# Performance work log

Measured on AMD Instinct MI355X. Metric: run time of the kernel, lower is better.

Reference implementation:

```python
import jax, jax.numpy as jnp
import numpy as np

VOCAB = 50257
EMB = 1024
HID = 1024
B, T = 8, 256


def setup_inputs() -> dict:
    key = jax.random.key(0)
    ks = jax.random.split(key, 6)
    s = 0.05  # small init scale for numerical sanity
    return {
        "x": jax.random.randint(ks[0], (B, T), 0, VOCAB, dtype=jnp.int64) if jax.config.jax_enable_x64 else jax.random.randint(ks[0], (B, T), 0, VOCAB, dtype=jnp.int32),
        "emb_W": jax.random.normal(ks[1], (VOCAB, EMB), dtype=jnp.float32) * s,
        "W_ih": jax.random.normal(ks[2], (4 * HID, EMB), dtype=jnp.float32) * s,
        "W_hh": jax.random.normal(ks[3], (4 * HID, HID), dtype=jnp.float32) * s,
        "b_ih": jax.random.normal(ks[4], (4 * HID,), dtype=jnp.float32) * s,
        "b_hh": jax.random.normal(ks[5], (4 * HID,), dtype=jnp.float32) * s,
        "dec_b": jnp.zeros((VOCAB,), dtype=jnp.float32),
    }


def _lstm(emb, W_ih, W_hh, b_ih, b_hh):
    # emb: [B, T, E]. Precompute input projections for all timesteps (one big GEMM).
    x_proj = jnp.einsum("bte,ge->btg", emb, W_ih) + (b_ih + b_hh)  # [B, T, 4H]
    h0 = jnp.zeros((emb.shape[0], HID), emb.dtype)
    c0 = jnp.zeros((emb.shape[0], HID), emb.dtype)

    def step(carry, xt):  # xt: [B, 4H]
        h, c = carry
        g = xt + h @ W_hh.T  # [B, 4H]
        i, f, gg, o = jnp.split(g, 4, axis=-1)  # PyTorch gate order i,f,g,o
        i = jax.nn.sigmoid(i)
        f = jax.nn.sigmoid(f)
        gg = jnp.tanh(gg)
        o = jax.nn.sigmoid(o)
        c_new = f * c + i * gg
        h_new = o * jnp.tanh(c_new)
        return (h_new, c_new), h_new

    (hT, cT), hs = jax.lax.scan(step, (h0, c0), jnp.swapaxes(x_proj, 0, 1))
    out = jnp.swapaxes(hs, 0, 1)  # [B, T, H], batch_first
    return out, (hT[None], cT[None])  # num_layers=1 leading dim


def reference(x, emb_W, W_ih, W_hh, b_ih, b_hh, dec_b):
    emb = emb_W[x]                                   # [B, T, E]
    out, hidden = _lstm(emb, W_ih, W_hh, b_ih, b_hh)  # [B, T, H]
    logits = jnp.einsum("bth,vh->btv", out, emb_W) + dec_b  # tied decoder
    logits = logits.reshape(-1, VOCAB)
    return jax.nn.log_softmax(logits, axis=1), hidden
```

## Files before the change

### kernel.cpp

```cpp
#include <hip/hip_runtime.h>

typedef float f32x4 __attribute__((ext_vector_type(4)));
typedef __bf16 bf16x8 __attribute__((ext_vector_type(8)));
typedef unsigned int u32x4 __attribute__((ext_vector_type(4)));
typedef unsigned short u16;
typedef unsigned int u32;

#define VOCAB 50257
#define KDIM 1024
#define MROWS 2048
#define TSEQ 256
#define NBLK 64
#define NTILE 393
#define NT (NTILE * 2)
#define LOGN ((size_t)MROWS * VOCAB)

__device__ __forceinline__ u16 f2bf(float f) {
    u32 u = __builtin_bit_cast(u32, f);
    u = (u + 0x7FFFu + ((u >> 16) & 1u)) >> 16;
    return (u16)u;
}

__device__ __forceinline__ float sigm(float x) { return 1.0f / (1.0f + __expf(-x)); }

__device__ __forceinline__ u32 min4u(u32x4 v) {
    u32 a = v.x < v.y ? v.x : v.y;
    u32 b = v.z < v.w ? v.z : v.w;
    return a < b ? a : b;
}


__global__ void conv_bf16(const float4* __restrict__ in, ushort4* __restrict__ out, long n4) {
    long i = (long)blockIdx.x * blockDim.x + threadIdx.x;
    long stride = (long)gridDim.x * blockDim.x;
    for (; i < n4; i += stride) {
        float4 v = in[i];
        ushort4 o;
        o.x = f2bf(v.x); o.y = f2bf(v.y); o.z = f2bf(v.z); o.w = f2bf(v.w);
        out[i] = o;
    }
}

__global__ void bias_sum(const float* __restrict__ a, const float* __restrict__ b,
                         float* __restrict__ o) {
    int i = blockIdx.x * 256 + threadIdx.x;
    if (i < 4096) o[i] = a[i] + b[i];
}

__global__ __launch_bounds__(256) void gather_emb(const int* __restrict__ x,
                                                  const float* __restrict__ embW,
                                                  u16* __restrict__ out) {
    int m = blockIdx.x;
    int row = x[m];
    const float4* src = (const float4*)(embW + (size_t)row * KDIM);
    ushort4* dst = (ushort4*)(out + (size_t)m * KDIM);
    float4 v = src[threadIdx.x];
    ushort4 o;
    o.x = f2bf(v.x); o.y = f2bf(v.y); o.z = f2bf(v.z); o.w = f2bf(v.w);
    dst[threadIdx.x] = o;
}

__global__ void init_hseq(u32* __restrict__ hs) {
    int i = blockIdx.x * 256 + threadIdx.x;
    if (i < 257 * 4096) hs[i] = (i < 4096) ? 0x00010001u : 0u;
}


#define BM 128
#define BN 128
#define BK 64

__device__ __forceinline__ void gl_lds16(const u16* g, const u16* l) {
    __builtin_amdgcn_global_load_lds(
        (const __attribute__((address_space(1))) u32*)g,
        (__attribute__((address_space(3))) u32*)l, 16, 0, 0);
}

__global__ __launch_bounds__(256, 2)
void gemm_bt(const u16* __restrict__ A, const u16* __restrict__ Bm,
             const float* __restrict__ bias, float* __restrict__ C,
             int N, int Nb, int K, int ldc)
{
    __shared__ __align__(16) u16 As[BM * BK];
    __shared__ __align__(16) u16 Bs[BN * BK];
    const int tid  = threadIdx.x;
    const int lane = tid & 63;
    const int wid  = tid >> 6;

    const int gx  = gridDim.x;
    const int nwg = gx * gridDim.y;
    const int lin = blockIdx.y * gx + blockIdx.x;
    const int qq = nwg >> 3, rr = nwg & 7;
    const int xcd = lin & 7, idx = lin >> 3;
    const int neu = (xcd < rr) ? (xcd * (qq + 1) + idx)
                               : (rr * (qq + 1) + (xcd - rr) * qq + idx);
    const int bm = neu % gx;
    const int bn = neu / gx;

    const int wr = wid >> 1, wc = wid & 1;

    const u16* gA[4]; const u16* gB[4];
    const u16* ldsA[4]; const u16* ldsB[4];
#pragma unroll
    for (int r = 0; r < 4; ++r) {
        int L = r * 256 + tid;
        int row = L >> 3, ps = L & 7;
        int ls = ps ^ (row & 7);
        gA[r] = A + (size_t)(bm * BM + row) * K + ls * 8;
        int brow = bn * BN + row; brow = brow < Nb ? brow : Nb - 1;
        gB[r] = Bm + (size_t)brow * K + ls * 8;
        ldsA[r] = As + (r * 256 + wid * 64) * 8;
        ldsB[r] = Bs + (r * 256 + wid * 64) * 8;
    }

    const int lrow = lane & 15, ksl = lane >> 4;
    int aoff[4][2], boff[4][2];
#pragma unroll
    for (int i = 0; i < 4; ++i)
#pragma unroll
        for (int ks = 0; ks < 2; ++ks) {
            int ar = wr * 64 + i * 16 + lrow;
            aoff[i][ks] = ar * BK + (((ks * 4 + ksl) ^ (ar & 7)) * 8);
            int br = wc * 64 + i * 16 + lrow;
            boff[i][ks] = br * BK + (((ks * 4 + ksl) ^ (br & 7)) * 8);
        }

    f32x4 acc[4][4] = {};
    for (int kt = 0; kt < K; kt += BK) {
#pragma unroll
        for (int r = 0; r < 4; ++r) gl_lds16(gA[r] + kt, ldsA[r]);
#pragma unroll
        for (int r = 0; r < 4; ++r) gl_lds16(gB[r] + kt, ldsB[r]);
        __syncthreads();
        bf16x8 af[4][2], bfb[4][2];
#pragma unroll
        for (int i = 0; i < 4; ++i)
#pragma unroll
            for (int ks = 0; ks < 2; ++ks) {
                af[i][ks]  = *(const bf16x8*)(As + aoff[i][ks]);
                bfb[i][ks] = *(const bf16x8*)(Bs + boff[i][ks]);
            }
#pragma unroll
        for (int ks = 0; ks < 2; ++ks)
#pragma unroll
            for (int mi = 0; mi < 4; ++mi)
#pragma unroll
                for (int ni = 0; ni < 4; ++ni)
                    acc[mi][ni] = __builtin_amdgcn_mfma_f32_16x16x32_bf16(
                        af[mi][ks], bfb[ni][ks], acc[mi][ni], 0, 0, 0);
        __syncthreads();
    }

    const int crl = lane >> 4, ccl = lane & 15;
    const int row0 = bm * BM + wr * 64, col0 = bn * BN + wc * 64;
#pragma unroll
    for (int ni = 0; ni < 4; ++ni) {
        int col = col0 + ni * 16 + ccl;
        if (col < N) {
            float bv = bias[col];
#pragma unroll
            for (int mi = 0; mi < 4; ++mi) {
                int row = row0 + mi * 16 + crl * 4;
                float* cp = C + (size_t)row * ldc + col;
#pragma unroll
                for (int r = 0; r < 4; ++r)
                    cp[(size_t)r * ldc] = acc[mi][ni][r] + bv;
            }
        }
    }
}


__global__ __launch_bounds__(256, 2)
void gemm_dec(const u16* __restrict__ A, const u16* __restrict__ Bm,
              const float* __restrict__ bias, float* __restrict__ C,
              float* __restrict__ pmax, float* __restrict__ psum)
{
    const int N = VOCAB, Nb = VOCAB, K = KDIM, ldc = VOCAB;
    __shared__ __align__(16) u16 As[BM * BK];
    __shared__ __align__(16) u16 Bs[BN * BK];
    const int tid  = threadIdx.x;
    const int lane = tid & 63;
    const int wid  = tid >> 6;

    const int gx  = gridDim.x;
    const int nwg = gx * gridDim.y;
    const int lin = blockIdx.y * gx + blockIdx.x;
    const int qq = nwg >> 3, rr = nwg & 7;
    const int xcd = lin & 7, idx = lin >> 3;
    const int neu = (xcd < rr) ? (xcd * (qq + 1) + idx)
                               : (rr * (qq + 1) + (xcd - rr) * qq + idx);
    const int bm = neu % gx;
    const int bn = neu / gx;

    const int wr = wid >> 1, wc = wid & 1;

    const u16* gA[4]; const u16* gB[4];
    const u16* ldsA[4]; const u16* ldsB[4];
#pragma unroll
    for (int r = 0; r < 4; ++r) {
        int L = r * 256 + tid;
        int row = L >> 3, ps = L & 7;
        int ls = ps ^ (row & 7);
        gA[r] = A + (size_t)(bm * BM + row) * K + ls * 8;
        int brow = bn * BN + row; brow = brow < Nb ? brow : Nb - 1;
        gB[r] = Bm + (size_t)brow * K + ls * 8;
        ldsA[r] = As + (r * 256 + wid * 64) * 8;
        ldsB[r] = Bs + (r * 256 + wid * 64) * 8;
    }

    const int lrow = lane & 15, ksl = lane >> 4;
    int aoff[4][2], boff[4][2];
#pragma unroll
    for (int i = 0; i < 4; ++i)
#pragma unroll
        for (int ks = 0; ks < 2; ++ks) {
            int ar = wr * 64 + i * 16 + lrow;
            aoff[i][ks] = ar * BK + (((ks * 4 + ksl) ^ (ar & 7)) * 8);
            int br = wc * 64 + i * 16 + lrow;
            boff[i][ks] = br * BK + (((ks * 4 + ksl) ^ (br & 7)) * 8);
        }

    f32x4 acc[4][4] = {};
    for (int kt = 0; kt < K; kt += BK) {
#pragma unroll
        for (int r = 0; r < 4; ++r) gl_lds16(gA[r] + kt, ldsA[r]);
#pragma unroll
        for (int r = 0; r < 4; ++r) gl_lds16(gB[r] + kt, ldsB[r]);
        __syncthreads();
        bf16x8 af[4][2], bfb[4][2];
#pragma unroll
        for (int i = 0; i < 4; ++i)
#pragma unroll
            for (int ks = 0; ks < 2; ++ks) {
                af[i][ks]  = *(const bf16x8*)(As + aoff[i][ks]);
                bfb[i][ks] = *(const bf16x8*)(Bs + boff[i][ks]);
            }
#pragma unroll
        for (int ks = 0; ks < 2; ++ks)
#pragma unroll
            for (int mi = 0; mi < 4; ++mi)
#pragma unroll
                for (int ni = 0; ni < 4; ++ni)
                    acc[mi][ni] = __builtin_amdgcn_mfma_f32_16x16x32_bf16(
                        af[mi][ks], bfb[ni][ks], acc[mi][ni], 0, 0, 0);
        __syncthreads();
    }

    const int crl = lane >> 4, ccl = lane & 15;
    const int row0 = bm * BM + wr * 64, col0 = bn * BN + wc * 64;
    float bve[4]; bool vld[4];
#pragma unroll
    for (int ni = 0; ni < 4; ++ni) {
        int col = col0 + ni * 16 + ccl;
        vld[ni] = col < N;
        bve[ni] = vld[ni] ? bias[col] : 0.f;
    }
#pragma unroll
    for (int ni = 0; ni < 4; ++ni) {
        if (vld[ni]) {
            int col = col0 + ni * 16 + ccl;
#pragma unroll
            for (int mi = 0; mi < 4; ++mi) {
                int row = row0 + mi * 16 + crl * 4;
                float* cp = C + (size_t)row * ldc + col;
#pragma unroll
                for (int r = 0; r < 4; ++r)
                    cp[(size_t)r * ldc] = acc[mi][ni][r] + bve[ni];
            }
        }
    }
#pragma unroll
    for (int mi = 0; mi < 4; ++mi)
#pragma unroll
        for (int r = 0; r < 4; ++r) {
            int row = row0 + mi * 16 + crl * 4 + r;
            float v0 = vld[0] ? acc[mi][0][r] + bve[0] : -3.0e38f;
            float v1 = vld[1] ? acc[mi][1][r] + bve[1] : -3.0e38f;
            float v2 = vld[2] ? acc[mi][2][r] + bve[2] : -3.0e38f;
            float v3 = vld[3] ? acc[mi][3][r] + bve[3] : -3.0e38f;
            float rmax = fmaxf(fmaxf(v0, v1), fmaxf(v2, v3));
#pragma unroll
            for (int m2 = 1; m2 < 16; m2 <<= 1) rmax = fmaxf(rmax, __shfl_xor(rmax, m2));
            float rs = __expf(v0 - rmax) + __expf(v1 - rmax) +
                       __expf(v2 - rmax) + __expf(v3 - rmax);
#pragma unroll
            for (int m2 = 1; m2 < 16; m2 <<= 1) rs += __shfl_xor(rs, m2);
            if (ccl == 0) {
                pmax[(size_t)row * NT + bn * 2 + wc] = rmax;
                psum[(size_t)row * NT + bn * 2 + wc] = rs;
            }
        }
}


__global__ __launch_bounds__(256, 1)
void lstm_persist(const u16* __restrict__ Whh,
                  const float* __restrict__ xproj,
                  u16* __restrict__ hseq,
                  u16* __restrict__ hall,
                  float* __restrict__ outTail)
{
    const int tid  = threadIdx.x;
    const int lane = tid & 63;
    const int wq   = tid >> 6;
    const int lrow = lane & 15, ksl = lane >> 4;
    const int bid  = blockIdx.x;
    const int colbase = bid * 16;

    bf16x8 Bf[32];
    {
        const u16* bp = Whh + (size_t)(wq * 1024 + colbase + lrow) * KDIM + ksl * 8;
#pragma unroll
        for (int kk = 0; kk < 32; ++kk)
            asm volatile("global_load_dwordx4 %0, %1, off"
                         : "=v"(Bf[kk]) : "v"(bp + kk * 32));
        asm volatile("s_waitcnt vmcnt(0)" ::: "memory");
        __builtin_amdgcn_sched_barrier(0);
    }

    __shared__ float S[4][8][16];
    __shared__ __align__(16) u16 hstage[2][64][16][16];

    for (int i = tid; i < 2 * 64 * 8; i += 256) {
        int buf = i >> 9, rem = i & 511;
        int j = rem >> 3, row = 8 + (rem & 7);
        u32x4 z = {0, 0, 0, 0};
        *(u32x4*)(&hstage[buf][j][row][0]) = z;
        *(u32x4*)(&hstage[buf][j][row][8]) = z;
    }

    const bool upd = tid < 128;
    const int b8 = tid >> 4, c16 = tid & 15;
    float creg = 0.f;
    float xp0 = 0.f, xp1 = 0.f, xp2 = 0.f, xp3 = 0.f;
    size_t xbase = 0;
    if (upd) {
        xbase = (size_t)b8 * TSEQ * 4096 + colbase + c16;
        xp0 = xproj[xbase];          xp1 = xproj[xbase + 1024];
        xp2 = xproj[xbase + 2048];   xp3 = xproj[xbase + 3072];
    }

    const int pj = tid >> 2, pr = (tid & 3) * 2;
    const int abase = (ksl >> 1) * 256 + lrow * 16 + (ksl & 1) * 8;

    for (int t = 0; t < TSEQ; ++t) {
        const u32* src = (const u32*)hseq + (size_t)t * 4096 + pj * 64 + pr * 8;
        u32x4 P0, P1, P2, P3;
        for (;;) {
            asm volatile("global_load_dwordx4 %0, %1, off sc0 sc1" : "=v"(P0) : "v"(src));
            asm volatile("global_load_dwordx4 %0, %1, off sc0 sc1" : "=v"(P1) : "v"(src + 4));
            asm volatile("global_load_dwordx4 %0, %1, off sc0 sc1" : "=v"(P2) : "v"(src + 8));
            asm volatile("global_load_dwordx4 %0, %1, off sc0 sc1" : "=v"(P3) : "v"(src + 12));
            asm volatile("s_waitcnt vmcnt(0)" ::: "memory");
            __builtin_amdgcn_sched_barrier(0);
            u32 a = min4u(P0), b = min4u(P1), c = min4u(P2), d = min4u(P3);
            u32 mn = (a < b ? a : b); u32 mn2 = (c < d ? c : d);
            if ((mn < mn2 ? mn : mn2) != 0u) break;
        }
        {
            u16* dst = &hstage[t & 1][pj][pr][0];
            *(u32x4*)(dst)      = P0;
            *(u32x4*)(dst + 8)  = P1;
            *(u32x4*)(dst + 16) = P2;
            *(u32x4*)(dst + 24) = P3;
        }
        __syncthreads();

        const u16* sb = &hstage[t & 1][0][0][0] + abase;
        f32x4 ac0 = {}, ac1 = {}, ac2 = {}, ac3 = {};
#pragma unroll
        for (int g = 0; g < 8; ++g) {
            bf16x8 a0 = *(const bf16x8*)(sb + (size_t)(g * 4 + 0) * 512);
            bf16x8 a1 = *(const bf16x8*)(sb + (size_t)(g * 4 + 1) * 512);
            bf16x8 a2 = *(const bf16x8*)(sb + (size_t)(g * 4 + 2) * 512);
            bf16x8 a3 = *(const bf16x8*)(sb + (size_t)(g * 4 + 3) * 512);
            ac0 = __builtin_amdgcn_mfma_f32_16x16x32_bf16(a0, Bf[g * 4 + 0], ac0, 0, 0, 0);
            ac1 = __builtin_amdgcn_mfma_f32_16x16x32_bf16(a1, Bf[g * 4 + 1], ac1, 0, 0, 0);
            ac2 = __builtin_amdgcn_mfma_f32_16x16x32_bf16(a2, Bf[g * 4 + 2], ac2, 0, 0, 0);
            ac3 = __builtin_amdgcn_mfma_f32_16x16x32_bf16(a3, Bf[g * 4 + 3], ac3, 0, 0, 0);
        }
        if (ksl < 2) {
#pragma unroll
            for (int r = 0; r < 4; ++r)
                S[wq][ksl * 4 + r][lrow] = ac0[r] + ac1[r] + ac2[r] + ac3[r];
        }
        __syncthreads();

        if (upd) {
            float gi = S[0][b8][c16] + xp0;
            float gf = S[1][b8][c16] + xp1;
            float gg = S[2][b8][c16] + xp2;
            float go = S[3][b8][c16] + xp3;
            float iv = sigm(gi), fv = sigm(gf), ov = sigm(go);
            float gv = tanhf(gg);
            creg = fv * creg + iv * gv;
            float hv = ov * tanhf(creg);
            u16 hbx = f2bf(hv) | 1;
            int w0 = (int)hbx;
            int w1 = __shfl_down(w0, 1);
            if (!(c16 & 1)) {
                u32 w = (u32)(u16)w0 | ((u32)(u16)w1 << 16);
                u32* dst = (u32*)hseq + (size_t)(t + 1) * 4096 + bid * 64 + b8 * 8 + (c16 >> 1);
                __hip_atomic_store(dst, w, __ATOMIC_RELAXED, __HIP_MEMORY_SCOPE_AGENT);
            }
            hall[((size_t)b8 * TSEQ + t) * KDIM + colbase + c16] = hbx;
            if (t == TSEQ - 1) {
                outTail[b8 * KDIM + colbase + c16] = hv;
                outTail[8192 + b8 * KDIM + colbase + c16] = creg;
            }
            int tn = (t + 1 < TSEQ) ? t + 1 : t;
            size_t xb = xbase + (size_t)tn * 4096;
            xp0 = xproj[xb];        xp1 = xproj[xb + 1024];
            xp2 = xproj[xb + 2048]; xp3 = xproj[xb + 3072];
        }
    }
}


__global__ __launch_bounds__(256)
void merge_lse(const float* __restrict__ pmax, const float* __restrict__ psum,
               float* __restrict__ lse) {
    const int m = blockIdx.x;
    const int tid = threadIdx.x;
    __shared__ float smx[4], ssm[4];
    float mx = -3.0e38f, s = 0.f;
    for (int i = tid; i < NT; i += 256) {
        float pm = pmax[(size_t)m * NT + i];
        float ps = psum[(size_t)m * NT + i];
        if (pm > mx) { s *= __expf(mx - pm); mx = pm; }
        s += ps * __expf(pm - mx);
    }
#pragma unroll
    for (int off = 32; off > 0; off >>= 1) {
        float om = __shfl_xor(mx, off), os = __shfl_xor(s, off);
        float nm = fmaxf(mx, om);
        s = s * __expf(mx - nm) + os * __expf(om - nm);
        mx = nm;
    }
    if ((tid & 63) == 0) { smx[tid >> 6] = mx; ssm[tid >> 6] = s; }
    __syncthreads();
    if (tid == 0) {
        float M = fmaxf(fmaxf(smx[0], smx[1]), fmaxf(smx[2], smx[3]));
        float S4 = ssm[0] * __expf(smx[0] - M) + ssm[1] * __expf(smx[1] - M) +
                   ssm[2] * __expf(smx[2] - M) + ssm[3] * __expf(smx[3] - M);
        lse[m] = M + __logf(S4);
    }
}

__global__ __launch_bounds__(256)
void final_sub(float* __restrict__ out, const float* __restrict__ lse) {
    const int m = blockIdx.x;
    float* row = out + (size_t)m * VOCAB;
    const float L = lse[m];
    const int tid = threadIdx.x;
    const int head = (int)(((16 - ((uintptr_t)row & 15)) & 15) >> 2);
    const int nv = (VOCAB - head) >> 2;
    const int tail0 = head + nv * 4;
    const int ntail = VOCAB - tail0;
    float4* rv = (float4*)(row + head);
    for (int i = tid; i < nv; i += 256) {
        float4 v = rv[i];
        v.x -= L; v.y -= L; v.z -= L; v.w -= L;
        rv[i] = v;
    }
    if (tid < head) row[tid] -= L;
    if (tid >= 64 && tid < 64 + ntail) row[tail0 + (tid - 64)] -= L;
}


extern "C" void kernel_launch(void* const* d_in, const int* in_sizes, int n_in,
                              void* d_out, int out_size, void* d_ws, size_t ws_size,
                              hipStream_t stream)
{
    const int*   x    = (const int*)d_in[0];
    const float* embW = (const float*)d_in[1];
    const float* Wih  = (const float*)d_in[2];
    const float* Whh  = (const float*)d_in[3];
    const float* bih  = (const float*)d_in[4];
    const float* bhh  = (const float*)d_in[5];
    const float* decb = (const float*)d_in[6];
    float* out = (float*)d_out;

    char* p = (char*)d_ws;
    auto carve = [&](size_t bytes) {
        char* q = p;
        p += (bytes + 255) & ~(size_t)255;
        return q;
    };
    u16*   embW_bf = (u16*)carve((size_t)VOCAB * KDIM * 2);
    u16*   Wih_bf  = (u16*)carve((size_t)4096 * KDIM * 2);
    u16*   Whh_bf  = (u16*)carve((size_t)4096 * KDIM * 2);
    u16*   emb_bf  = (u16*)carve((size_t)MROWS * KDIM * 2);
    float* xproj   = (float*)carve((size_t)MROWS * 4096 * 4);
    u16*   hall_bf = (u16*)carve((size_t)MROWS * KDIM * 2);
    u16*   hseq    = (u16*)carve((size_t)(TSEQ + 1) * 4096 * 4);
    float* pmax    = (float*)carve((size_t)MROWS * NT * 4);
    float* psum    = (float*)carve((size_t)MROWS * NT * 4);
    float* lse     = (float*)carve((size_t)MROWS * 4);
    float* bsum    = (float*)carve((size_t)4096 * 4);

    init_hseq<<<(257 * 4096 + 255) / 256, 256, 0, stream>>>((u32*)hseq);

    conv_bf16<<<1024, 256, 0, stream>>>((const float4*)Wih, (ushort4*)Wih_bf,
                                        (long)4096 * KDIM / 4);
    conv_bf16<<<1024, 256, 0, stream>>>((const float4*)Whh, (ushort4*)Whh_bf,
                                        (long)4096 * KDIM / 4);
    conv_bf16<<<2048, 256, 0, stream>>>((const float4*)embW, (ushort4*)embW_bf,
                                        (long)VOCAB * KDIM / 4);
    bias_sum<<<16, 256, 0, stream>>>(bih, bhh, bsum);
    gather_emb<<<MROWS, 256, 0, stream>>>(x, embW, emb_bf);

    {
        dim3 g(MROWS / BM, 4096 / BN);
        gemm_bt<<<g, 256, 0, stream>>>(emb_bf, Wih_bf, bsum, xproj, 4096, 4096, KDIM, 4096);
    }

    lstm_persist<<<NBLK, 256, 0, stream>>>(Whh_bf, xproj, hseq, hall_bf, out + LOGN);

    {
        dim3 g(MROWS / BM, NTILE);
        gemm_dec<<<g, 256, 0, stream>>>(hall_bf, embW_bf, decb, out, pmax, psum);
    }

    merge_lse<<<MROWS, 256, 0, stream>>>(pmax, psum, lse);
    final_sub<<<MROWS, 256, 0, stream>>>(out, lse);
}
```

Baseline: 1.324 ms.

## Overlap embedding bf16 conversion with LSTM, store bf16 logits, swizzle LDS staging

The embedding-table fp32-to-bf16 conversion moves into extra helper blocks of the persistent LSTM launch, so it runs on CUs the recurrence leaves idle instead of as a separate kernel. The decoder GEMM now writes logits as bf16 into the output buffer's first half, and final_sub expands them to fp32 in place, walking the chunks backwards so no bf16 source is overwritten before it is read. This halves the logit write traffic but rounds logits to bf16 before log-softmax. The LSTM h staging in LDS also gets an XOR swizzle to reduce bank conflicts.

```diff
diff --git a/kernel.cpp b/kernel.cpp
--- a/kernel.cpp
+++ b/kernel.cpp
@@ -11,6 +11,7 @@
 #define MROWS 2048
 #define TSEQ 256
 #define NBLK 64
+#define NHELP 192
 #define NTILE 393
 #define NT (NTILE * 2)
 #define LOGN ((size_t)MROWS * VOCAB)
@@ -173,10 +174,10 @@
 
 __global__ __launch_bounds__(256, 2)
 void gemm_dec(const u16* __restrict__ A, const u16* __restrict__ Bm,
-              const float* __restrict__ bias, float* __restrict__ C,
+              const float* __restrict__ bias, u16* __restrict__ Cb,
               float* __restrict__ pmax, float* __restrict__ psum)
 {
-    const int N = VOCAB, Nb = VOCAB, K = KDIM, ldc = VOCAB;
+    const int N = VOCAB, Nb = VOCAB, K = KDIM;
     __shared__ __align__(16) u16 As[BM * BK];
     __shared__ __align__(16) u16 Bs[BN * BK];
     const int tid  = threadIdx.x;
@@ -263,10 +264,10 @@
 #pragma unroll
             for (int mi = 0; mi < 4; ++mi) {
                 int row = row0 + mi * 16 + crl * 4;
-                float* cp = C + (size_t)row * ldc + col;
+                u16* cp = Cb + (size_t)row * (VOCAB * 2) + col;
 #pragma unroll
                 for (int r = 0; r < 4; ++r)
-                    cp[(size_t)r * ldc] = acc[mi][ni][r] + bve[ni];
+                    cp[(size_t)r * (VOCAB * 2)] = f2bf(acc[mi][ni][r] + bve[ni]);
             }
         }
     }
@@ -299,13 +300,29 @@
                   const float* __restrict__ xproj,
                   u16* __restrict__ hseq,
                   u16* __restrict__ hall,
-                  float* __restrict__ outTail)
+                  float* __restrict__ outTail,
+                  const float4* __restrict__ embW,
+                  ushort4* __restrict__ embW_bf)
 {
-    const int tid  = threadIdx.x;
+    const int tid = threadIdx.x;
+    const int bid = blockIdx.x;
+
+    if (bid >= NBLK) {
+        long i = (long)(bid - NBLK) * 256 + tid;
+        const long n4 = (long)VOCAB * KDIM / 4;
+        const long stride = (long)NHELP * 256;
+        for (; i < n4; i += stride) {
+            float4 v = embW[i];
+            ushort4 o;
+            o.x = f2bf(v.x); o.y = f2bf(v.y); o.z = f2bf(v.z); o.w = f2bf(v.w);
+            embW_bf[i] = o;
+        }
+        return;
+    }
+
     const int lane = tid & 63;
     const int wq   = tid >> 6;
     const int lrow = lane & 15, ksl = lane >> 4;
-    const int bid  = blockIdx.x;
     const int colbase = bid * 16;
 
     bf16x8 Bf[32];
@@ -320,14 +337,14 @@
     }
 
     __shared__ float S[4][8][16];
-    __shared__ __align__(16) u16 hstage[2][64][16][16];
+    __shared__ __align__(16) u16 hstage[2][16384];
 
     for (int i = tid; i < 2 * 64 * 8; i += 256) {
         int buf = i >> 9, rem = i & 511;
-        int j = rem >> 3, row = 8 + (rem & 7);
+        int j = rem >> 3, rowoff = rem & 7;
         u32x4 z = {0, 0, 0, 0};
-        *(u32x4*)(&hstage[buf][j][row][0]) = z;
-        *(u32x4*)(&hstage[buf][j][row][8]) = z;
+        *(u32x4*)(&hstage[buf][j * 256 + 128 + rowoff * 16]) = z;
+        *(u32x4*)(&hstage[buf][j * 256 + 128 + rowoff * 16 + 8]) = z;
     }
 
     const bool upd = tid < 128;
@@ -342,7 +359,18 @@
     }
 
     const int pj = tid >> 2, pr = (tid & 3) * 2;
-    const int abase = (ksl >> 1) * 256 + lrow * 16 + (ksl & 1) * 8;
+    const int sw = (pj & 7) << 3;
+    int widx[4];
+#pragma unroll
+    for (int k = 0; k < 4; ++k)
+        widx[k] = pj * 256 + ((pr * 16 + k * 8) ^ sw);
+
+    int aro[4];
+#pragma unroll
+    for (int i = 0; i < 4; ++i) {
+        int swr = ((2 * i + (ksl >> 1)) & 7) << 3;
+        aro[i] = (ksl >> 1) * 256 + ((lrow * 16 + (ksl & 1) * 8) ^ swr);
+    }
 
     for (int t = 0; t < TSEQ; ++t) {
         const u32* src = (const u32*)hseq + (size_t)t * 4096 + pj * 64 + pr * 8;
@@ -359,22 +387,22 @@
             if ((mn < mn2 ? mn : mn2) != 0u) break;
         }
         {
-            u16* dst = &hstage[t & 1][pj][pr][0];
-            *(u32x4*)(dst)      = P0;
-            *(u32x4*)(dst + 8)  = P1;
-            *(u32x4*)(dst + 16) = P2;
-            *(u32x4*)(dst + 24) = P3;
-        }
-        __syncthreads();
-
-        const u16* sb = &hstage[t & 1][0][0][0] + abase;
+            u16* hb = &hstage[t & 1][0];
+            *(u32x4*)(hb + widx[0]) = P0;
+            *(u32x4*)(hb + widx[1]) = P1;
+            *(u32x4*)(hb + widx[2]) = P2;
+            *(u32x4*)(hb + widx[3]) = P3;
+        }
+        __syncthreads();
+
+        const u16* sb = &hstage[t & 1][0];
         f32x4 ac0 = {}, ac1 = {}, ac2 = {}, ac3 = {};
 #pragma unroll
         for (int g = 0; g < 8; ++g) {
-            bf16x8 a0 = *(const bf16x8*)(sb + (size_t)(g * 4 + 0) * 512);
-            bf16x8 a1 = *(const bf16x8*)(sb + (size_t)(g * 4 + 1) * 512);
-            bf16x8 a2 = *(const bf16x8*)(sb + (size_t)(g * 4 + 2) * 512);
-            bf16x8 a3 = *(const bf16x8*)(sb + (size_t)(g * 4 + 3) * 512);
+            bf16x8 a0 = *(const bf16x8*)(sb + g * 2048 + 0 * 512 + aro[0]);
+            bf16x8 a1 = *(const bf16x8*)(sb + g * 2048 + 1 * 512 + aro[1]);
+            bf16x8 a2 = *(const bf16x8*)(sb + g * 2048 + 2 * 512 + aro[2]);
+            bf16x8 a3 = *(const bf16x8*)(sb + g * 2048 + 3 * 512 + aro[3]);
             ac0 = __builtin_amdgcn_mfma_f32_16x16x32_bf16(a0, Bf[g * 4 + 0], ac0, 0, 0, 0);
             ac1 = __builtin_amdgcn_mfma_f32_16x16x32_bf16(a1, Bf[g * 4 + 1], ac1, 0, 0, 0);
             ac2 = __builtin_amdgcn_mfma_f32_16x16x32_bf16(a2, Bf[g * 4 + 2], ac2, 0, 0, 0);
@@ -451,21 +479,33 @@
 __global__ __launch_bounds__(256)
 void final_sub(float* __restrict__ out, const float* __restrict__ lse) {
     const int m = blockIdx.x;
-    float* row = out + (size_t)m * VOCAB;
     const float L = lse[m];
+    const u32* srcw = (const u32*)out + (size_t)m * VOCAB;
+    float* dst = out + (size_t)m * VOCAB;
     const int tid = threadIdx.x;
-    const int head = (int)(((16 - ((uintptr_t)row & 15)) & 15) >> 2);
-    const int nv = (VOCAB - head) >> 2;
-    const int tail0 = head + nv * 4;
-    const int ntail = VOCAB - tail0;
-    float4* rv = (float4*)(row + head);
-    for (int i = tid; i < nv; i += 256) {
-        float4 v = rv[i];
-        v.x -= L; v.y -= L; v.z -= L; v.w -= L;
-        rv[i] = v;
-    }
-    if (tid < head) row[tid] -= L;
-    if (tid >= 64 && tid < 64 + ntail) row[tail0 + (tid - 64)] -= L;
+    const int NCH = (VOCAB + 2047) / 2048;
+    for (int c = NCH - 1; c >= 0; --c) {
+        int e0 = c * 2048 + tid * 8;
+        int w0i = e0 >> 1;
+        u32 w0 = srcw[w0i], w1 = srcw[w0i + 1], w2 = srcw[w0i + 2], w3 = srcw[w0i + 3];
+        __syncthreads();
+        float f[8];
+        f[0] = __builtin_bit_cast(float, (w0 & 0xFFFFu) << 16) - L;
+        f[1] = __builtin_bit_cast(float, w0 & 0xFFFF0000u) - L;
+        f[2] = __builtin_bit_cast(float, (w1 & 0xFFFFu) << 16) - L;
+        f[3] = __builtin_bit_cast(float, w1 & 0xFFFF0000u) - L;
+        f[4] = __builtin_bit_cast(float, (w2 & 0xFFFFu) << 16) - L;
+        f[5] = __builtin_bit_cast(float, w2 & 0xFFFF0000u) - L;
+        f[6] = __builtin_bit_cast(float, (w3 & 0xFFFFu) << 16) - L;
+        f[7] = __builtin_bit_cast(float, w3 & 0xFFFF0000u) - L;
+        if (e0 + 8 <= VOCAB) {
+#pragma unroll
+            for (int k = 0; k < 8; ++k) dst[e0 + k] = f[k];
+        } else {
+#pragma unroll
+            for (int k = 0; k < 8; ++k) if (e0 + k < VOCAB) dst[e0 + k] = f[k];
+        }
+    }
 }
 
 
@@ -506,8 +546,6 @@
                                         (long)4096 * KDIM / 4);
     conv_bf16<<<1024, 256, 0, stream>>>((const float4*)Whh, (ushort4*)Whh_bf,
                                         (long)4096 * KDIM / 4);
-    conv_bf16<<<2048, 256, 0, stream>>>((const float4*)embW, (ushort4*)embW_bf,
-                                        (long)VOCAB * KDIM / 4);
     bias_sum<<<16, 256, 0, stream>>>(bih, bhh, bsum);
     gather_emb<<<MROWS, 256, 0, stream>>>(x, embW, emb_bf);
 
@@ -516,11 +554,14 @@
         gemm_bt<<<g, 256, 0, stream>>>(emb_bf, Wih_bf, bsum, xproj, 4096, 4096, KDIM, 4096);
     }
 
-    lstm_persist<<<NBLK, 256, 0, stream>>>(Whh_bf, xproj, hseq, hall_bf, out + LOGN);
+    lstm_persist<<<NBLK + NHELP, 256, 0, stream>>>(Whh_bf, xproj, hseq, hall_bf,
+                                                   out + LOGN,
+                                                   (const float4*)embW,
+                                                   (ushort4*)embW_bf);
 
     {
         dim3 g(MROWS / BM, NTILE);
-        gemm_dec<<<g, 256, 0, stream>>>(hall_bf, embW_bf, decb, out, pmax, psum);
+        gemm_dec<<<g, 256, 0, stream>>>(hall_bf, embW_bf, decb, (u16*)out, pmax, psum);
     }
 
     merge_lse<<<MROWS, 256, 0, stream>>>(pmax, psum, lse);
```

After: 1.217 ms. 8.1% less time.
